# Kernel tuning notes

Hardware: AMD Instinct MI355X
Metric: run time of the kernel (lower is better)

## Reference

```python
import jax, jax.numpy as jnp
import numpy as np
from jax import lax

KS = 3      # generated depthwise kernel size
F = 9       # utils.FILTERS (channels)
P = 24      # utils.PSZ (patch size); conv stride 8 -> KS = P/8


def _extract_patches(x, p):
    # TF extract_patches with sizes=strides=p, VALID: (B,H,W,C) -> (B,nh,nw,p*p*C)
    B, H, W, C = x.shape
    nh, nw = H // p, W // p
    return (x.reshape(B, nh, p, nw, p, C)
             .transpose(0, 1, 3, 2, 4, 5)
             .reshape(B, nh, nw, p * p * C))


def setup_inputs() -> dict:
    key = jax.random.key(0)
    ks = jax.random.split(key, 6)
    B, H, Wd = 16, 384, 384
    return {
        "guidance": jax.random.normal(ks[0], (B, H, Wd, F), jnp.float32),
        "depth": jax.random.normal(ks[1], (B, H, Wd, F), jnp.float32),
        "conv_w": jax.random.normal(ks[2], (KS, KS, F, 9), jnp.float32) * 0.05,
        "conv_b": jax.random.normal(ks[3], (9,), jnp.float32) * 0.05,
        "dense_w": jax.random.normal(ks[4], (F, F * F), jnp.float32) * 0.05,
        "dense_b": jax.random.normal(ks[5], (F * F,), jnp.float32) * 0.05,
    }


def _forward(guidance, depth, conv_w, conv_b, dense_w, dense_b):
    B, H, W, _ = guidance.shape
    NP = (H // P) * (W // P)
    NB = NP * B
    # raw TF reshape (B,nh,nw,P*P*F) -> (NP,B,P,P,F), reproduced faithfully
    gp = _extract_patches(guidance, P).reshape(NP, B, P, P, F)
    dp = _extract_patches(depth, P).reshape(NP, B, P, P, F)

    # --- KGL: per-patch kernel generation (vectorized over NP*B) ---
    gflat = gp.reshape(NB, P, P, F)
    c = lax.conv_general_dilated(gflat, conv_w, (8, 8), 'SAME',
                                 dimension_numbers=('NHWC', 'HWIO', 'NHWC')) + conv_b
    W_G1 = c.reshape(NP, B, KS, KS, F, 1)
    n1 = jnp.sqrt(jnp.sum(W_G1 * W_G1, axis=(2, 3), keepdims=True))
    W_G1 = W_G1 / jnp.maximum(n1, 1.0)          # tf.clip_by_norm(.., 1, axes=[1,2])

    gap = gp.mean(axis=(2, 3))                   # (NP,B,F)
    d = gap @ dense_w + dense_b                  # (NP,B,F*F)
    W_G2 = d.reshape(NP, B, 1, 1, F, F)
    n2 = jnp.sqrt(jnp.sum(W_G2 * W_G2, axis=(2, 3, 4), keepdims=True))
    W_G2 = W_G2 / jnp.maximum(n2, 1.0)           # clip_by_norm axes=[1,2,3]

    # --- per-sample dynamic depthwise conv (vmap over NP*B) ---
    dw_rhs = W_G1.reshape(NB, KS, KS, F, 1).transpose(0, 1, 2, 4, 3)  # HWIO, groups=F
    dflat = dp.reshape(NB, P, P, F)

    def dwconv(img, f):
        return lax.conv_general_dilated(img[None], f, (1, 1), 'SAME',
                                        dimension_numbers=('NHWC', 'HWIO', 'NHWC'),
                                        feature_group_count=F)[0]

    dc = jax.vmap(dwconv)(dflat, dw_rhs)         # (NB,P,P,F)

    # --- per-sample dynamic 1x1 cross-channel conv == matmul ---
    cc = jnp.einsum('npqi,nio->npqo', dc, W_G2.reshape(NB, F, F))
    # raw TF reshape (NP,B,P,P,F) -> (B,H,W,F), reproduced faithfully
    return cc.reshape(B, H, W, F)


def reference(guidance, depth, conv_w, conv_b, dense_w, dense_b):
    return _forward(guidance, depth, conv_w, conv_b, dense_w, dense_b)
```

## Files before the change

### kernel.cpp

```cpp
#include <hip/hip_runtime.h>
#include <stdint.h>


__device__ __forceinline__ void gload16(const float* gsrc, float* ldst) {
    __builtin_amdgcn_global_load_lds(
        (__attribute__((address_space(1))) void*)gsrc,
        (__attribute__((address_space(3))) void*)ldst, 16, 0, 0);
}

__global__ __launch_bounds__(576, 6) void fused_kernel(
    const float* __restrict__ g,
    const float* __restrict__ dep,
    const float* __restrict__ cw,
    const float* __restrict__ cb,
    const float* __restrict__ dw,
    const float* __restrict__ db,
    float* __restrict__ out)
{
    __shared__ __align__(16) float sg[5184];
    __shared__ __align__(16) float sd[5184];
    __shared__ __align__(16) float cwf[729];
    __shared__ __align__(16) float dwf[729];
    __shared__ float cbf[9];
    __shared__ float dbf[81];
    __shared__ float cols[216];
    __shared__ float gapm[9];
    __shared__ float cful[81];
    __shared__ __align__(16) float sw[216];

    const int m = blockIdx.x;
    const int t = threadIdx.x;
    const int b0 = m >> 8, pi = (m >> 4) & 15, pj = m & 15;
    const long rowbase = ((long)(b0 * 384 + pi * 24)) * 3456 + (long)pj * 216;

    for (int task = t; task < 1296; task += 576) {
        int r = task / 54, c4 = task - r * 54;
        gload16(g + rowbase + (long)r * 3456 + c4 * 4, sg + task * 4);
    }
    for (int task = t; task < 1296; task += 576) {
        int r = task / 54, c4 = task - r * 54;
        gload16(dep + rowbase + (long)r * 3456 + c4 * 4, sd + task * 4);
    }
    for (int idx = t; idx < 729; idx += 576) { cwf[idx] = cw[idx]; dwf[idx] = dw[idx]; }
    if (t < 9) cbf[t] = cb[t];
    if (t >= 64 && t < 145) dbf[t - 64] = db[t - 64];
    __syncthreads();

    if (t < 216) {
        float s = 0.f;
        #pragma unroll
        for (int r = 0; r < 24; ++r) s += sg[r * 216 + t];
        cols[t] = s;
    } else if (t >= 256 && t < 337) {
        const int q = t - 256;
        const int o = q % 9, uv = q / 9, v = uv % 3, u = uv / 3;
        float acc = cbf[o];
        #pragma unroll
        for (int du = 0; du < 3; ++du)
        #pragma unroll
        for (int dv = 0; dv < 3; ++dv) {
            const float* gp2 = &sg[(u * 8 + du) * 216 + (v * 8 + dv) * 9];
            const float* wp  = &cwf[(du * 3 + dv) * 81 + o];
            #pragma unroll
            for (int ci = 0; ci < 9; ++ci) acc += gp2[ci] * wp[ci * 9];
        }
        cful[q] = acc;
    }
    __syncthreads();

    if (t < 9) {
        float s = 0.f;
        #pragma unroll
        for (int c = 0; c < 24; ++c) s += cols[c * 9 + t];
        gapm[t] = s * (1.0f / 576.0f);
    } else if (t >= 64 && t < 73) {
        const int f = t - 64;
        float s = 0.f;
        #pragma unroll
        for (int k = 0; k < 9; ++k) { float c = cful[k * 9 + f]; s += c * c; }
        const float scale = (s > 1.0f) ? (1.0f / sqrtf(s)) : 1.0f;
        #pragma unroll
        for (int k = 0; k < 9; ++k) sw[k * 12 + f] = cful[k * 9 + f] * scale;
    }
    __syncthreads();

    if (t < 9) {
        float gv[9];
        #pragma unroll
        for (int k = 0; k < 9; ++k) gv[k] = gapm[k];
        float d[9];
        float s = 0.f;
        #pragma unroll
        for (int i = 0; i < 9; ++i) {
            float a = dbf[i * 9 + t];
            #pragma unroll
            for (int k = 0; k < 9; ++k) a += gv[k] * dwf[k * 81 + i * 9 + t];
            d[i] = a; s += a * a;
        }
        const float scale = (s > 1.0f) ? (1.0f / sqrtf(s)) : 1.0f;
        #pragma unroll
        for (int i = 0; i < 9; ++i) sw[108 + t * 12 + i] = d[i] * scale;
    }
    __syncthreads();

    {
        const int row = t / 24;
        const int col = t - row * 24;
        float dc[9];
        #pragma unroll
        for (int i = 0; i < 9; ++i) dc[i] = 0.f;

        #pragma unroll
        for (int du = 0; du < 3; ++du) {
            const int r = row + du - 1;
            if (r < 0 || r > 23) continue;
            #pragma unroll
            for (int dv = 0; dv < 3; ++dv) {
                const int c = col + dv - 1;
                if (c < 0 || c > 23) continue;
                const float* sp = &sd[r * 216 + c * 9];
                const float* wv = &sw[(du * 3 + dv) * 12];
                #pragma unroll
                for (int i = 0; i < 9; ++i) dc[i] += sp[i] * wv[i];
            }
        }

        float* op = out + (long)m * 5184 + t * 9;
        #pragma unroll
        for (int o = 0; o < 9; ++o) {
            const float* wv = &sw[108 + o * 12];
            float a = 0.f;
            #pragma unroll
            for (int i = 0; i < 9; ++i) a += dc[i] * wv[i];
            op[o] = a;
        }
    }
}

extern "C" void kernel_launch(void* const* d_in, const int* in_sizes, int n_in,
                              void* d_out, int out_size, void* d_ws, size_t ws_size,
                              hipStream_t stream) {
    const float* g  = (const float*)d_in[0];
    const float* dp = (const float*)d_in[1];
    const float* cw = (const float*)d_in[2];
    const float* cb = (const float*)d_in[3];
    const float* dw = (const float*)d_in[4];
    const float* db = (const float*)d_in[5];
    float* out = (float*)d_out;
    (void)d_ws; (void)ws_size;

    fused_kernel<<<dim3(4096), dim3(576), 0, stream>>>(g, dp, cw, cb, dw, db, out);
}
```

Before: 237.9 us.

## Make blocks persistent over several patches and prefetch next patch into registers

The grid shrinks from one block per patch to 768 persistent blocks, each handling 5–6 patches. The next patch's guidance and depth are prefetched into registers while the current one is computed. Guidance no longer goes to LDS in full: only a register partial sum for the mean and a compacted 9x9 sample for the strided conv are stored. Conv weights are transposed once per block, and barriers become raw lgkmcnt waits plus s_barrier. The aim is to overlap global loads with compute and amortise weight setup, at the cost of more registers and possible load imbalance across the 5- and 6-patch blocks.

New measurement: 467.0 us. 1.96x slower.

```diff
diff --git a/kernel.cpp b/kernel.cpp
--- a/kernel.cpp
+++ b/kernel.cpp
@@ -2,13 +2,15 @@
 #include <stdint.h>
 
 
-__device__ __forceinline__ void gload16(const float* gsrc, float* ldst) {
-    __builtin_amdgcn_global_load_lds(
-        (__attribute__((address_space(1))) void*)gsrc,
-        (__attribute__((address_space(3))) void*)ldst, 16, 0, 0);
+#define LGKM0_BAR() \
+    asm volatile("s_waitcnt lgkmcnt(0)\n\ts_barrier" ::: "memory")
+
+__device__ __forceinline__ long patch_rowbase(int m) {
+    const int b0 = m >> 8, pi = (m >> 4) & 15, pj = m & 15;
+    return ((long)(b0 * 384 + pi * 24)) * 3456 + (long)pj * 216;
 }
 
-__global__ __launch_bounds__(576, 6) void fused_kernel(
+__global__ __launch_bounds__(576, 7) void fused_kernel(
     const float* __restrict__ g,
     const float* __restrict__ dep,
     const float* __restrict__ cw,
@@ -17,123 +19,167 @@
     const float* __restrict__ db,
     float* __restrict__ out)
 {
-    __shared__ __align__(16) float sg[5184];
-    __shared__ __align__(16) float sd[5184];
-    __shared__ __align__(16) float cwf[729];
-    __shared__ __align__(16) float dwf[729];
+    __shared__ __align__(16) float sdep[5184];
+    __shared__ __align__(16) float part2[576];
+    __shared__ __align__(16) float sw[216];
+    __shared__ float cwT[729];
+    __shared__ float dwf[729];
+    __shared__ float scratch[729];
     __shared__ float cbf[9];
     __shared__ float dbf[81];
-    __shared__ float cols[216];
     __shared__ float gapm[9];
     __shared__ float cful[81];
-    __shared__ __align__(16) float sw[216];
 
-    const int m = blockIdx.x;
-    const int t = threadIdx.x;
-    const int b0 = m >> 8, pi = (m >> 4) & 15, pj = m & 15;
-    const long rowbase = ((long)(b0 * 384 + pi * 24)) * 3456 + (long)pj * 216;
+    const int bk = blockIdx.x;
+    const int t  = threadIdx.x;
+    int p0, np;
+    if (bk < 256) { p0 = bk * 6;                np = 6; }
+    else          { p0 = 1536 + (bk - 256) * 5; np = 5; }
 
-    for (int task = t; task < 1296; task += 576) {
-        int r = task / 54, c4 = task - r * 54;
-        gload16(g + rowbase + (long)r * 3456 + c4 * 4, sg + task * 4);
+    for (int idx = t; idx < 729; idx += 576) {
+        const int uv = idx / 81, rem = idx - uv * 81, o = rem / 9, ci = rem - o * 9;
+        cwT[idx] = cw[uv * 81 + ci * 9 + o];
+        dwf[idx] = dw[idx];
     }
-    for (int task = t; task < 1296; task += 576) {
-        int r = task / 54, c4 = task - r * 54;
-        gload16(dep + rowbase + (long)r * 3456 + c4 * 4, sd + task * 4);
-    }
-    for (int idx = t; idx < 729; idx += 576) { cwf[idx] = cw[idx]; dwf[idx] = dw[idx]; }
     if (t < 9) cbf[t] = cb[t];
     if (t >= 64 && t < 145) dbf[t - 64] = db[t - 64];
     __syncthreads();
 
-    if (t < 216) {
-        float s = 0.f;
+    float gn[9], dn[9];
+    {
+        const long rb = patch_rowbase(p0);
         #pragma unroll
-        for (int r = 0; r < 24; ++r) s += sg[r * 216 + t];
-        cols[t] = s;
-    } else if (t >= 256 && t < 337) {
-        const int q = t - 256;
-        const int o = q % 9, uv = q / 9, v = uv % 3, u = uv / 3;
-        float acc = cbf[o];
-        #pragma unroll
-        for (int du = 0; du < 3; ++du)
-        #pragma unroll
-        for (int dv = 0; dv < 3; ++dv) {
-            const float* gp2 = &sg[(u * 8 + du) * 216 + (v * 8 + dv) * 9];
-            const float* wp  = &cwf[(du * 3 + dv) * 81 + o];
+        for (int k = 0; k < 9; ++k) {
+            const int idx = t + 576 * k;
+            const int r = idx / 216;
+            const long a = rb + idx + (long)r * 3240;
+            gn[k] = g[a];
+            dn[k] = dep[a];
+        }
+    }
+
+    for (int it = 0; it < np; ++it) {
+        const int m = p0 + it;
+
+        {
+            float s = 0.f;
             #pragma unroll
-            for (int ci = 0; ci < 9; ++ci) acc += gp2[ci] * wp[ci * 9];
-        }
-        cful[q] = acc;
-    }
-    __syncthreads();
-
-    if (t < 9) {
-        float s = 0.f;
-        #pragma unroll
-        for (int c = 0; c < 24; ++c) s += cols[c * 9 + t];
-        gapm[t] = s * (1.0f / 576.0f);
-    } else if (t >= 64 && t < 73) {
-        const int f = t - 64;
-        float s = 0.f;
-        #pragma unroll
-        for (int k = 0; k < 9; ++k) { float c = cful[k * 9 + f]; s += c * c; }
-        const float scale = (s > 1.0f) ? (1.0f / sqrtf(s)) : 1.0f;
-        #pragma unroll
-        for (int k = 0; k < 9; ++k) sw[k * 12 + f] = cful[k * 9 + f] * scale;
-    }
-    __syncthreads();
-
-    if (t < 9) {
-        float gv[9];
-        #pragma unroll
-        for (int k = 0; k < 9; ++k) gv[k] = gapm[k];
-        float d[9];
-        float s = 0.f;
-        #pragma unroll
-        for (int i = 0; i < 9; ++i) {
-            float a = dbf[i * 9 + t];
+            for (int k = 0; k < 9; ++k) s += gn[k];
+            part2[t] = s;
             #pragma unroll
-            for (int k = 0; k < 9; ++k) a += gv[k] * dwf[k * 81 + i * 9 + t];
-            d[i] = a; s += a * a;
-        }
-        const float scale = (s > 1.0f) ? (1.0f / sqrtf(s)) : 1.0f;
-        #pragma unroll
-        for (int i = 0; i < 9; ++i) sw[108 + t * 12 + i] = d[i] * scale;
-    }
-    __syncthreads();
-
-    {
-        const int row = t / 24;
-        const int col = t - row * 24;
-        float dc[9];
-        #pragma unroll
-        for (int i = 0; i < 9; ++i) dc[i] = 0.f;
-
-        #pragma unroll
-        for (int du = 0; du < 3; ++du) {
-            const int r = row + du - 1;
-            if (r < 0 || r > 23) continue;
+            for (int k = 0; k < 9; ++k) sdep[t + 576 * k] = dn[k];
+            const int ch = t % 9;
             #pragma unroll
-            for (int dv = 0; dv < 3; ++dv) {
-                const int c = col + dv - 1;
-                if (c < 0 || c > 23) continue;
-                const float* sp = &sd[r * 216 + c * 9];
-                const float* wv = &sw[(du * 3 + dv) * 12];
-                #pragma unroll
-                for (int i = 0; i < 9; ++i) dc[i] += sp[i] * wv[i];
+            for (int k = 0; k < 9; ++k) {
+                const int idx = t + 576 * k;
+                const int r = idx / 216, x = idx - r * 216;
+                const int c = x / 9;
+                if (((r & 7) < 3) && ((c & 7) < 3)) {
+                    const int ri  = (r >> 3) * 3 + (r & 7);
+                    const int ci2 = (c >> 3) * 3 + (c & 7);
+                    scratch[(ri * 9 + ci2) * 9 + ch] = gn[k];
+                }
             }
         }
 
-        float* op = out + (long)m * 5184 + t * 9;
-        #pragma unroll
-        for (int o = 0; o < 9; ++o) {
-            const float* wv = &sw[108 + o * 12];
-            float a = 0.f;
+        if (it + 1 < np) {
+            const long rb = patch_rowbase(m + 1);
             #pragma unroll
-            for (int i = 0; i < 9; ++i) a += dc[i] * wv[i];
-            op[o] = a;
+            for (int k = 0; k < 9; ++k) {
+                const int idx = t + 576 * k;
+                const int r = idx / 216;
+                const long a = rb + idx + (long)r * 3240;
+                gn[k] = g[a];
+                dn[k] = dep[a];
+            }
         }
+        LGKM0_BAR();
+
+        if (t < 81) {
+            const int o = t % 9, uv = t / 9, v = uv % 3, u = uv / 3;
+            float acc = cbf[o];
+            #pragma unroll
+            for (int du = 0; du < 3; ++du)
+            #pragma unroll
+            for (int dv = 0; dv < 3; ++dv) {
+                const float* sp = &scratch[((u * 3 + du) * 9 + (v * 3 + dv)) * 9];
+                const float* wp = &cwT[(du * 3 + dv) * 81 + o * 9];
+                #pragma unroll
+                for (int ci = 0; ci < 9; ++ci) acc += sp[ci] * wp[ci];
+            }
+            cful[t] = acc;
+        } else if (t >= 128 && t < 137) {
+            const int c = t - 128;
+            float s = 0.f;
+            #pragma unroll
+            for (int j = 0; j < 64; ++j) s += part2[j * 9 + c];
+            gapm[c] = s * (1.0f / 576.0f);
+        }
+        LGKM0_BAR();
+
+        if (t < 9) {
+            float gv[9];
+            #pragma unroll
+            for (int k = 0; k < 9; ++k) gv[k] = gapm[k];
+            float dvals[9]; float ss = 0.f;
+            #pragma unroll
+            for (int i = 0; i < 9; ++i) {
+                float a = dbf[i * 9 + t];
+                #pragma unroll
+                for (int k = 0; k < 9; ++k) a += gv[k] * dwf[k * 81 + i * 9 + t];
+                dvals[i] = a; ss += a * a;
+            }
+            const float sc2 = (ss > 1.0f) ? (1.0f / sqrtf(ss)) : 1.0f;
+            #pragma unroll
+            for (int i = 0; i < 9; ++i) sw[108 + t * 12 + i] = dvals[i] * sc2;
+        } else if (t >= 64 && t < 73) {
+            const int f = t - 64;
+            float ss = 0.f;
+            #pragma unroll
+            for (int k = 0; k < 9; ++k) { const float cc = cful[k * 9 + f]; ss += cc * cc; }
+            const float sc1 = (ss > 1.0f) ? (1.0f / sqrtf(ss)) : 1.0f;
+            #pragma unroll
+            for (int k = 0; k < 9; ++k) sw[k * 12 + f] = cful[k * 9 + f] * sc1;
+        }
+        LGKM0_BAR();
+
+        {
+            const int row = t / 24, col = t - row * 24;
+            float dc[9];
+            #pragma unroll
+            for (int i = 0; i < 9; ++i) dc[i] = 0.f;
+
+            #pragma unroll
+            for (int du = 0; du < 3; ++du) {
+                const int r = row + du - 1;
+                if (r < 0 || r > 23) continue;
+                #pragma unroll
+                for (int dv = 0; dv < 3; ++dv) {
+                    const int c = col + dv - 1;
+                    if (c < 0 || c > 23) continue;
+                    const float* sp = &sdep[(r * 24 + c) * 9];
+                    const float* wb = &sw[(du * 3 + dv) * 12];
+                    const float4 W0 = *reinterpret_cast<const float4*>(wb);
+                    const float4 W1 = *reinterpret_cast<const float4*>(wb + 4);
+                    const float w8 = wb[8];
+                    dc[0] += sp[0] * W0.x; dc[1] += sp[1] * W0.y; dc[2] += sp[2] * W0.z;
+                    dc[3] += sp[3] * W0.w; dc[4] += sp[4] * W1.x; dc[5] += sp[5] * W1.y;
+                    dc[6] += sp[6] * W1.z; dc[7] += sp[7] * W1.w; dc[8] += sp[8] * w8;
+                }
+            }
+
+            float* op = out + (long)m * 5184 + t * 9;
+            #pragma unroll
+            for (int o = 0; o < 9; ++o) {
+                const float* wb = &sw[108 + o * 12];
+                const float4 W0 = *reinterpret_cast<const float4*>(wb);
+                const float4 W1 = *reinterpret_cast<const float4*>(wb + 4);
+                op[o] = dc[0] * W0.x + dc[1] * W0.y + dc[2] * W0.z + dc[3] * W0.w
+                      + dc[4] * W1.x + dc[5] * W1.y + dc[6] * W1.z + dc[7] * W1.w
+                      + dc[8] * wb[8];
+            }
+        }
+        LGKM0_BAR();
     }
 }
 
@@ -149,5 +195,5 @@
     float* out = (float*)d_out;
     (void)d_ws; (void)ws_size;
 
-    fused_kernel<<<dim3(4096), dim3(576), 0, stream>>>(g, dp, cw, cb, dw, db, out);
+    fused_kernel<<<dim3(768), dim3(576), 0, stream>>>(g, dp, cw, cb, dw, db, out);
 }
```

## Shrink block to 256 threads, share one LDS buffer, stage depth via registers

Applied to the files above, without the earlier changes.

Reduces the block from 576 to 256 threads, with each thread handling two or three output pixels. The guidance and depth patches now share a single LDS buffer: depth is prefetched into registers during the guidance phase and written to LDS once the guidance reductions are finished. The dense weights and biases are read straight from global memory rather than staged in LDS, and the stages are reordered. The aim is to cut LDS use per block so more blocks fit per CU, at the cost of more registers per thread and extra work per thread.

New measurement: 295.1 us. +24.0%, slower.

```diff
diff --git a/kernel.cpp b/kernel.cpp
--- a/kernel.cpp
+++ b/kernel.cpp
@@ -8,7 +8,42 @@
         (__attribute__((address_space(3))) void*)ldst, 16, 0, 0);
 }
 
-__global__ __launch_bounds__(576, 6) void fused_kernel(
+__device__ __forceinline__ void do_pixel(const float* __restrict__ sd,
+                                         const float* __restrict__ sw,
+                                         float* __restrict__ out, int p) {
+    const int row = p / 24;
+    const int col = p - row * 24;
+    float dc[9];
+    #pragma unroll
+    for (int i = 0; i < 9; ++i) dc[i] = 0.f;
+
+    #pragma unroll
+    for (int du = 0; du < 3; ++du) {
+        const int r = row + du - 1;
+        if (r < 0 || r > 23) continue;
+        #pragma unroll
+        for (int dv = 0; dv < 3; ++dv) {
+            const int c = col + dv - 1;
+            if (c < 0 || c > 23) continue;
+            const float* sp = &sd[(r * 24 + c) * 9];
+            const float* wv = &sw[(du * 3 + dv) * 12];
+            #pragma unroll
+            for (int i = 0; i < 9; ++i) dc[i] += sp[i] * wv[i];
+        }
+    }
+
+    float* op = out + p * 9;
+    #pragma unroll
+    for (int o = 0; o < 9; ++o) {
+        const float* wv = &sw[108 + o * 12];
+        float a = 0.f;
+        #pragma unroll
+        for (int i = 0; i < 9; ++i) a += dc[i] * wv[i];
+        op[o] = a;
+    }
+}
+
+__global__ __launch_bounds__(256, 6) void fused_kernel(
     const float* __restrict__ g,
     const float* __restrict__ dep,
     const float* __restrict__ cw,
@@ -17,123 +52,107 @@
     const float* __restrict__ db,
     float* __restrict__ out)
 {
-    __shared__ __align__(16) float sg[5184];
-    __shared__ __align__(16) float sd[5184];
-    __shared__ __align__(16) float cwf[729];
-    __shared__ __align__(16) float dwf[729];
-    __shared__ float cbf[9];
-    __shared__ float dbf[81];
+    __shared__ __align__(16) float buf[5184];
+    __shared__ float cwf[729];
     __shared__ float cols[216];
+    __shared__ __align__(16) float sw[216];
     __shared__ float gapm[9];
     __shared__ float cful[81];
-    __shared__ __align__(16) float sw[216];
 
     const int m = blockIdx.x;
     const int t = threadIdx.x;
     const int b0 = m >> 8, pi = (m >> 4) & 15, pj = m & 15;
     const long rowbase = ((long)(b0 * 384 + pi * 24)) * 3456 + (long)pj * 216;
 
-    for (int task = t; task < 1296; task += 576) {
+    for (int idx = t; idx < 729; idx += 256) cwf[idx] = cw[idx];
+    for (int task = t; task < 1296; task += 256) {
         int r = task / 54, c4 = task - r * 54;
-        gload16(g + rowbase + (long)r * 3456 + c4 * 4, sg + task * 4);
+        gload16(g + rowbase + (long)r * 3456 + c4 * 4, buf + task * 4);
     }
-    for (int task = t; task < 1296; task += 576) {
-        int r = task / 54, c4 = task - r * 54;
-        gload16(dep + rowbase + (long)r * 3456 + c4 * 4, sd + task * 4);
+    float4 dreg[6];
+    #pragma unroll
+    for (int k = 0; k < 5; ++k) {
+        const int task = t + 256 * k;
+        const int r = task / 54, c4 = task - r * 54;
+        dreg[k] = *reinterpret_cast<const float4*>(dep + rowbase + (long)r * 3456 + c4 * 4);
     }
-    for (int idx = t; idx < 729; idx += 576) { cwf[idx] = cw[idx]; dwf[idx] = dw[idx]; }
-    if (t < 9) cbf[t] = cb[t];
-    if (t >= 64 && t < 145) dbf[t - 64] = db[t - 64];
+    if (t < 16) {
+        const int task = t + 1280;
+        const int r = task / 54, c4 = task - r * 54;
+        dreg[5] = *reinterpret_cast<const float4*>(dep + rowbase + (long)r * 3456 + c4 * 4);
+    }
+    float cbv = 0.f;
+    if (t < 81) cbv = cb[t % 9];
     __syncthreads();
 
     if (t < 216) {
         float s = 0.f;
         #pragma unroll
-        for (int r = 0; r < 24; ++r) s += sg[r * 216 + t];
+        for (int r = 0; r < 24; ++r) s += buf[r * 216 + t];
         cols[t] = s;
-    } else if (t >= 256 && t < 337) {
-        const int q = t - 256;
-        const int o = q % 9, uv = q / 9, v = uv % 3, u = uv / 3;
-        float acc = cbf[o];
+    }
+    __syncthreads();
+
+    if (t < 81) {
+        const int o = t % 9, uv = t / 9, v = uv % 3, u = uv / 3;
+        float acc = cbv;
         #pragma unroll
         for (int du = 0; du < 3; ++du)
         #pragma unroll
         for (int dv = 0; dv < 3; ++dv) {
-            const float* gp2 = &sg[(u * 8 + du) * 216 + (v * 8 + dv) * 9];
+            const float* gp2 = &buf[(u * 8 + du) * 216 + (v * 8 + dv) * 9];
             const float* wp  = &cwf[(du * 3 + dv) * 81 + o];
             #pragma unroll
             for (int ci = 0; ci < 9; ++ci) acc += gp2[ci] * wp[ci * 9];
         }
-        cful[q] = acc;
+        cful[t] = acc;
+    } else if (t >= 96 && t < 105) {
+        const int c = t - 96;
+        float s = 0.f;
+        #pragma unroll
+        for (int j = 0; j < 24; ++j) s += cols[j * 9 + c];
+        gapm[c] = s * (1.0f / 576.0f);
     }
     __syncthreads();
 
+    {
+        float4* b4 = reinterpret_cast<float4*>(buf);
+        #pragma unroll
+        for (int k = 0; k < 5; ++k) b4[t + 256 * k] = dreg[k];
+        if (t < 16) b4[t + 1280] = dreg[5];
+    }
     if (t < 9) {
-        float s = 0.f;
+        float gv[9];
         #pragma unroll
-        for (int c = 0; c < 24; ++c) s += cols[c * 9 + t];
-        gapm[t] = s * (1.0f / 576.0f);
+        for (int k = 0; k < 9; ++k) gv[k] = gapm[k];
+        float d[9];
+        float ss = 0.f;
+        #pragma unroll
+        for (int i = 0; i < 9; ++i) {
+            float a = db[i * 9 + t];
+            #pragma unroll
+            for (int k = 0; k < 9; ++k) a += gv[k] * dw[k * 81 + i * 9 + t];
+            d[i] = a; ss += a * a;
+        }
+        const float scale = (ss > 1.0f) ? (1.0f / sqrtf(ss)) : 1.0f;
+        #pragma unroll
+        for (int i = 0; i < 9; ++i) sw[108 + t * 12 + i] = d[i] * scale;
     } else if (t >= 64 && t < 73) {
         const int f = t - 64;
-        float s = 0.f;
+        float ss = 0.f;
         #pragma unroll
-        for (int k = 0; k < 9; ++k) { float c = cful[k * 9 + f]; s += c * c; }
-        const float scale = (s > 1.0f) ? (1.0f / sqrtf(s)) : 1.0f;
+        for (int k = 0; k < 9; ++k) { const float c = cful[k * 9 + f]; ss += c * c; }
+        const float scale = (ss > 1.0f) ? (1.0f / sqrtf(ss)) : 1.0f;
         #pragma unroll
         for (int k = 0; k < 9; ++k) sw[k * 12 + f] = cful[k * 9 + f] * scale;
     }
     __syncthreads();
 
-    if (t < 9) {
-        float gv[9];
-        #pragma unroll
-        for (int k = 0; k < 9; ++k) gv[k] = gapm[k];
-        float d[9];
-        float s = 0.f;
-        #pragma unroll
-        for (int i = 0; i < 9; ++i) {
-            float a = dbf[i * 9 + t];
-            #pragma unroll
-            for (int k = 0; k < 9; ++k) a += gv[k] * dwf[k * 81 + i * 9 + t];
-            d[i] = a; s += a * a;
-        }
-        const float scale = (s > 1.0f) ? (1.0f / sqrtf(s)) : 1.0f;
-        #pragma unroll
-        for (int i = 0; i < 9; ++i) sw[108 + t * 12 + i] = d[i] * scale;
-    }
-    __syncthreads();
-
     {
-        const int row = t / 24;
-        const int col = t - row * 24;
-        float dc[9];
-        #pragma unroll
-        for (int i = 0; i < 9; ++i) dc[i] = 0.f;
-
-        #pragma unroll
-        for (int du = 0; du < 3; ++du) {
-            const int r = row + du - 1;
-            if (r < 0 || r > 23) continue;
-            #pragma unroll
-            for (int dv = 0; dv < 3; ++dv) {
-                const int c = col + dv - 1;
-                if (c < 0 || c > 23) continue;
-                const float* sp = &sd[r * 216 + c * 9];
-                const float* wv = &sw[(du * 3 + dv) * 12];
-                #pragma unroll
-                for (int i = 0; i < 9; ++i) dc[i] += sp[i] * wv[i];
-            }
-        }
-
-        float* op = out + (long)m * 5184 + t * 9;
-        #pragma unroll
-        for (int o = 0; o < 9; ++o) {
-            const float* wv = &sw[108 + o * 12];
-            float a = 0.f;
-            #pragma unroll
-            for (int i = 0; i < 9; ++i) a += dc[i] * wv[i];
-            op[o] = a;
-        }
+        float* ob = out + (long)m * 5184;
+        do_pixel(buf, sw, ob, t);
+        do_pixel(buf, sw, ob, t + 256);
+        if (t < 64) do_pixel(buf, sw, ob, t + 512);
     }
 }
 
@@ -149,5 +168,5 @@
     float* out = (float*)d_out;
     (void)d_ws; (void)ws_size;
 
-    fused_kernel<<<dim3(4096), dim3(576), 0, stream>>>(g, dp, cw, cb, dw, db, out);
+    fused_kernel<<<dim3(4096), dim3(256), 0, stream>>>(g, dp, cw, cb, dw, db, out);
 }
```
